# Kernel optimization log

Hardware: AMD Instinct MI355X
Metric: run time of the kernel (lower is better)

## Reference

```python
import jax, jax.numpy as jnp
import numpy as np

B, T, I, H, O = 256, 256, 128, 512, 1


def setup_inputs() -> dict:
    key = jax.random.key(0)
    ks = jax.random.split(key, 7)
    s = 1.0 / np.sqrt(H)  # torch default uniform-ish scale, use scaled normal
    return {
        "x": jax.random.normal(ks[0], (B, T, I), jnp.float32),
        "W_ih": jax.random.normal(ks[1], (H, I), jnp.float32) * s,
        "W_hh": jax.random.normal(ks[2], (H, H), jnp.float32) * s,
        "b_ih": jax.random.normal(ks[3], (H,), jnp.float32) * s,
        "b_hh": jax.random.normal(ks[4], (H,), jnp.float32) * s,
        "fc_w": jax.random.normal(ks[5], (O, H), jnp.float32) * s,
        "fc_b": jax.random.normal(ks[6], (O,), jnp.float32) * s,
    }


def reference(x, W_ih, W_hh, b_ih, b_hh, fc_w, fc_b):
    # Elman RNN (tanh), batch_first, h0 = 0; fc applied to last-step hidden.
    # Precompute all input projections in one big GEMM: [T, B, H]
    xs = jnp.einsum('bti,hi->tbh', x, W_ih) + (b_ih + b_hh)

    def step(h, xt):  # h: [B, H], xt: [B, H]
        h = jnp.tanh(xt + h @ W_hh.T)
        return h, None

    h0 = jnp.zeros((x.shape[0], W_hh.shape[0]), x.dtype)
    hT, _ = jax.lax.scan(step, h0, xs)
    return hT @ fc_w.T + fc_b  # [B, O]
```

## Files before the change

### kernel.cpp

```cpp
#include <hip/hip_runtime.h>


#define B_   256
#define T_   256
#define I_   128
#define H_   512

typedef __attribute__((ext_vector_type(8))) short short8;
typedef __attribute__((ext_vector_type(4))) float f32x4;

static __device__ inline unsigned short f2bf(float f) {
    union { float f; unsigned u; } v; v.f = f;
    unsigned r = v.u + 0x7fffu + ((v.u >> 16) & 1u);
    return (unsigned short)(r >> 16);
}
static __device__ inline float bf2f(unsigned short s) {
    union { unsigned u; float f; } v; v.u = ((unsigned)s) << 16;
    return v.f;
}
static __device__ inline float fast_tanh(float x) {
    float e = __expf(2.0f * x);
    float r = __builtin_amdgcn_rcpf(e + 1.0f);
    return __builtin_fmaf(-2.0f, r, 1.0f);
}
static __device__ inline short8 pack8(float4 lo, float4 hi) {
    short8 v;
    v[0] = (short)f2bf(lo.x); v[1] = (short)f2bf(lo.y);
    v[2] = (short)f2bf(lo.z); v[3] = (short)f2bf(lo.w);
    v[4] = (short)f2bf(hi.x); v[5] = (short)f2bf(hi.y);
    v[6] = (short)f2bf(hi.z); v[7] = (short)f2bf(hi.w);
    return v;
}

#define NKC   16
#define RS2  520
#define KC_LDS 3
#define KC_REG 3
#define KC_STR 10

__global__ void pack_w16(const float* __restrict__ W_hh,
                         unsigned short* __restrict__ Bpack) {
    int idx = blockIdx.x * blockDim.x + threadIdx.x;
    if (idx >= 32 * NKC * 64) return;
    int lane = idx & 63;
    int kc   = (idx >> 6) % NKC;
    int nt   = (idx >> 6) / NKC;
    int n  = nt * 16 + (lane & 15);
    int k0 = kc * 32 + (lane >> 4) * 8;
    unsigned short* dst = Bpack + (size_t)idx * 8;
#pragma unroll
    for (int e = 0; e < 8; ++e)
        dst[e] = f2bf(W_hh[n * H_ + k0 + e]);
}

__global__ __launch_bounds__(256)
void xproj_k(const float* __restrict__ x,
             const float* __restrict__ W_ih,
             const float* __restrict__ b_ih,
             const float* __restrict__ b_hh,
             unsigned short* __restrict__ xp) {
    const int tid  = threadIdx.x;
    const int lane = tid & 63;
    const int w    = tid >> 6;
    const int mr   = lane & 15;
    const int q    = lane >> 4;
    const int t0   = blockIdx.x * 4;
    const int bg   = blockIdx.y;

    short8 bf[4][4];
    const float* xb = x + (size_t)(16 * bg + mr) * T_ * I_ + q * 8;
#pragma unroll
    for (int tt = 0; tt < 4; ++tt)
#pragma unroll
        for (int kc = 0; kc < 4; ++kc) {
            const float* p = xb + (size_t)(t0 + tt) * I_ + kc * 32;
            bf[tt][kc] = pack8(*(const float4*)(p), *(const float4*)(p + 4));
        }

#pragma unroll
    for (int mt = 0; mt < 8; ++mt) {
        const int nrow = w * 128 + mt * 16 + mr;
        f32x4 a[4];
#pragma unroll
        for (int tt = 0; tt < 4; ++tt) a[tt] = (f32x4)(0.0f);
#pragma unroll
        for (int kc = 0; kc < 4; ++kc) {
            const float* ab = W_ih + (size_t)nrow * I_ + kc * 32 + q * 8;
            short8 af = pack8(*(const float4*)(ab), *(const float4*)(ab + 4));
#pragma unroll
            for (int tt = 0; tt < 4; ++tt)
                a[tt] = __builtin_amdgcn_mfma_f32_16x16x32_bf16(af, bf[tt][kc], a[tt], 0, 0, 0);
        }
#pragma unroll
        for (int tt = 0; tt < 4; ++tt) {
            unsigned short* dst = xp + ((size_t)((t0 + tt) * 16 + bg) * 512) * 16;
#pragma unroll
            for (int e = 0; e < 4; ++e) {
                int n = w * 128 + mt * 16 + q * 4 + e;
                float bv = b_ih[n] + b_hh[n];
                dst[(size_t)n * 16 + mr] = f2bf(a[tt][e] + bv);
            }
        }
    }
}

__global__ __launch_bounds__(512)
void rnn_fast(const unsigned short* __restrict__ Bpack,
              const unsigned short* __restrict__ xp,
              const float* __restrict__ fc_w,
              const float* __restrict__ fc_b,
              float* __restrict__ out) {
    __shared__ __align__(16) unsigned short a_lds[2][16 * RS2];
    __shared__ __align__(16) unsigned short w_lds[32 * KC_LDS * 64 * 8];

    const int tid  = threadIdx.x;
    const int lane = tid & 63;
    const int w    = tid >> 6;
    const int q    = lane >> 4;
    const int mr   = lane & 15;
    const int blk  = blockIdx.x;
    const int bb   = blk * 16;

    for (int i = tid; i < 16 * RS2; i += 512) a_lds[0][i] = 0;

    for (int i = tid; i < 32 * KC_LDS * 64; i += 512) {
        int l  = i & 63;
        int kc = (i >> 6) % KC_LDS;
        int nt = (i >> 6) / KC_LDS;
        *(short8*)&w_lds[(size_t)i * 8] =
            *(const short8*)(Bpack + ((size_t)(nt * NKC + kc) * 64 + l) * 8);
    }

    short8 wreg[KC_REG][4];
#pragma unroll
    for (int r = 0; r < KC_REG; ++r)
#pragma unroll
        for (int j = 0; j < 4; ++j)
            wreg[r][j] = *(const short8*)(Bpack +
                ((size_t)((4 * w + j) * NKC + KC_LDS + r) * 64 + lane) * 8);
#pragma unroll
    for (int r = 0; r < KC_REG; ++r)
#pragma unroll
        for (int j = 0; j < 4; ++j)
            asm volatile("" : "+v"(wreg[r][j]));

    __syncthreads();

    f32x4 acc[4];
    short8 sb[3][4];

    const unsigned short* xpt = xp + ((size_t)blk * 512) * 16;
    const size_t xstride = (size_t)16 * 512 * 16;

    for (int t = 0; t < T_; ++t) {
        const unsigned short* A = a_lds[t & 1];
        unsigned short* An      = a_lds[(t & 1) ^ 1];

#pragma unroll
        for (int s = 0; s < 3; ++s)
#pragma unroll
            for (int j = 0; j < 4; ++j)
                sb[s][j] = *(const short8*)(Bpack +
                    ((size_t)((4 * w + j) * NKC + KC_LDS + KC_REG + s) * 64 + lane) * 8);

        ushort4 xpr[4];
#pragma unroll
        for (int j = 0; j < 4; ++j) {
            int col = (4 * w + j) * 16 + mr;
            xpr[j] = *(const ushort4*)(xpt + (size_t)col * 16 + q * 4);
        }

#pragma unroll
        for (int j = 0; j < 4; ++j) acc[j] = (f32x4)(0.0f);

#pragma unroll
        for (int kc = 0; kc < KC_LDS; ++kc) {
            short8 af = *(const short8*)&A[mr * RS2 + kc * 32 + q * 8];
#pragma unroll
            for (int j = 0; j < 4; ++j) {
                short8 bfr = *(const short8*)&w_lds[
                    (size_t)(((4 * w + j) * KC_LDS + kc) * 64 + lane) * 8];
                acc[j] = __builtin_amdgcn_mfma_f32_16x16x32_bf16(af, bfr, acc[j], 0, 0, 0);
            }
        }
#pragma unroll
        for (int r = 0; r < KC_REG; ++r) {
            short8 af = *(const short8*)&A[mr * RS2 + (KC_LDS + r) * 32 + q * 8];
#pragma unroll
            for (int j = 0; j < 4; ++j)
                acc[j] = __builtin_amdgcn_mfma_f32_16x16x32_bf16(af, wreg[r][j], acc[j], 0, 0, 0);
        }
#pragma unroll
        for (int s = 0; s < KC_STR; ++s) {
            int kc = KC_LDS + KC_REG + s;
            short8 af = *(const short8*)&A[mr * RS2 + kc * 32 + q * 8];
#pragma unroll
            for (int j = 0; j < 4; ++j)
                acc[j] = __builtin_amdgcn_mfma_f32_16x16x32_bf16(af, sb[s % 3][j], acc[j], 0, 0, 0);
            if (s + 3 < KC_STR) {
#pragma unroll
                for (int j = 0; j < 4; ++j)
                    sb[s % 3][j] = *(const short8*)(Bpack +
                        ((size_t)((4 * w + j) * NKC + kc + 3) * 64 + lane) * 8);
            }
        }

#pragma unroll
        for (int j = 0; j < 4; ++j) {
            int col = (4 * w + j) * 16 + mr;
            const unsigned short* xj = (const unsigned short*)&xpr[j];
#pragma unroll
            for (int e = 0; e < 4; ++e) {
                float hv = fast_tanh(acc[j][e] + bf2f(xj[e]));
                An[(q * 4 + e) * RS2 + col] = f2bf(hv);
            }
        }
        xpt += xstride;
        __syncthreads();
    }

    {
        const int row = tid >> 5;
        const int l32 = tid & 31;
        float s = 0.0f;
        for (int k = l32; k < H_; k += 32)
            s += bf2f(a_lds[0][row * RS2 + k]) * fc_w[k];
#pragma unroll
        for (int off = 16; off > 0; off >>= 1)
            s += __shfl_down(s, off, 32);
        if (l32 == 0) out[bb + row] = s + fc_b[0];
    }
}

#define FB_NKC   20
#define FB_NKC_H 16
#define FB_RS   648
#define FB_KC_LDS 4
#define FB_KC_REG 5
#define FB_KC_STR 7

__global__ void pack_w20(const float* __restrict__ W_ih,
                         const float* __restrict__ W_hh,
                         unsigned short* __restrict__ Bpack) {
    int idx = blockIdx.x * blockDim.x + threadIdx.x;
    if (idx >= 32 * FB_NKC * 64) return;
    int lane = idx & 63;
    int kc   = (idx >> 6) % FB_NKC;
    int nt   = (idx >> 6) / FB_NKC;
    int n  = nt * 16 + (lane & 15);
    int k0 = kc * 32 + (lane >> 4) * 8;
    unsigned short* dst = Bpack + (size_t)idx * 8;
#pragma unroll
    for (int e = 0; e < 8; ++e) {
        int k = k0 + e;
        float v = (k < H_) ? W_hh[n * H_ + k] : W_ih[n * I_ + (k - H_)];
        dst[e] = f2bf(v);
    }
}

__global__ __launch_bounds__(512, 2)
void rnn_fb(const float* __restrict__ x,
            const unsigned short* __restrict__ Bpack,
            const float* __restrict__ b_ih,
            const float* __restrict__ b_hh,
            const float* __restrict__ fc_w,
            const float* __restrict__ fc_b,
            float* __restrict__ out) {
    __shared__ __align__(16) unsigned short a_lds[16 * FB_RS];
    __shared__ __align__(16) unsigned short w_lds[32 * FB_KC_LDS * 64 * 8];

    const int tid  = threadIdx.x;
    const int lane = tid & 63;
    const int w    = tid >> 6;
    const int q    = lane >> 4;
    const int mr   = lane & 15;
    const int bb   = blockIdx.x * 16;

    for (int i = tid; i < 16 * FB_RS; i += 512) a_lds[i] = 0;

    for (int i = tid; i < 32 * FB_KC_LDS * 64; i += 512) {
        int l  = i & 63;
        int kc = (i >> 6) & (FB_KC_LDS - 1);
        int nt = i >> 8;
        *(short8*)&w_lds[(size_t)i * 8] =
            *(const short8*)(Bpack + ((size_t)(nt * FB_NKC + kc) * 64 + l) * 8);
    }

    float bias[4];
#pragma unroll
    for (int j = 0; j < 4; ++j) {
        int col = (4 * w + j) * 16 + mr;
        bias[j] = b_ih[col] + b_hh[col];
    }

    short8 wih[4][4];
#pragma unroll
    for (int j = 0; j < 4; ++j)
#pragma unroll
        for (int kx = 0; kx < 4; ++kx)
            wih[j][kx] = *(const short8*)(Bpack +
                ((size_t)((4 * w + j) * FB_NKC + FB_NKC_H + kx) * 64 + lane) * 8);

    short8 wreg[FB_KC_REG][4];
#pragma unroll
    for (int r = 0; r < FB_KC_REG; ++r)
#pragma unroll
        for (int j = 0; j < 4; ++j)
            wreg[r][j] = *(const short8*)(Bpack +
                ((size_t)((4 * w + j) * FB_NKC + FB_KC_LDS + r) * 64 + lane) * 8);

    const int xrow = tid >> 5;
    const int xc   = (tid & 31) * 4;
    const float* xbase = x + (size_t)(bb + xrow) * T_ * I_ + xc;
    float4 xreg = *(const float4*)(xbase);

    __syncthreads();

    f32x4 acc[4];
    short8 sb[3][4];

    for (int t = 0; t < T_; ++t) {
#pragma unroll
        for (int s = 0; s < 3; ++s)
#pragma unroll
            for (int j = 0; j < 4; ++j)
                sb[s][j] = *(const short8*)(Bpack +
                    ((size_t)((4 * w + j) * FB_NKC + FB_KC_LDS + FB_KC_REG + s) * 64 + lane) * 8);

        {
            ushort4 xs;
            xs.x = f2bf(xreg.x); xs.y = f2bf(xreg.y);
            xs.z = f2bf(xreg.z); xs.w = f2bf(xreg.w);
            *(ushort4*)&a_lds[xrow * FB_RS + H_ + xc] = xs;
        }
        __syncthreads();

        if (t + 1 < T_)
            xreg = *(const float4*)(xbase + (size_t)(t + 1) * I_);

#pragma unroll
        for (int j = 0; j < 4; ++j) acc[j] = (f32x4)(0.0f);

#pragma unroll
        for (int kc = 0; kc < FB_KC_LDS; ++kc) {
            short8 af = *(const short8*)&a_lds[mr * FB_RS + kc * 32 + q * 8];
#pragma unroll
            for (int j = 0; j < 4; ++j) {
                short8 bfr = *(const short8*)&w_lds[
                    (size_t)(((4 * w + j) * FB_KC_LDS + kc) * 64 + lane) * 8];
                acc[j] = __builtin_amdgcn_mfma_f32_16x16x32_bf16(af, bfr, acc[j], 0, 0, 0);
            }
        }
#pragma unroll
        for (int r = 0; r < FB_KC_REG; ++r) {
            short8 af = *(const short8*)&a_lds[mr * FB_RS + (FB_KC_LDS + r) * 32 + q * 8];
#pragma unroll
            for (int j = 0; j < 4; ++j)
                acc[j] = __builtin_amdgcn_mfma_f32_16x16x32_bf16(af, wreg[r][j], acc[j], 0, 0, 0);
        }
#pragma unroll
        for (int kx = 0; kx < 4; ++kx) {
            short8 af = *(const short8*)&a_lds[mr * FB_RS + H_ + kx * 32 + q * 8];
#pragma unroll
            for (int j = 0; j < 4; ++j)
                acc[j] = __builtin_amdgcn_mfma_f32_16x16x32_bf16(af, wih[j][kx], acc[j], 0, 0, 0);
        }
#pragma unroll
        for (int s = 0; s < FB_KC_STR; ++s) {
            int kc = FB_KC_LDS + FB_KC_REG + s;
            short8 af = *(const short8*)&a_lds[mr * FB_RS + kc * 32 + q * 8];
#pragma unroll
            for (int j = 0; j < 4; ++j)
                acc[j] = __builtin_amdgcn_mfma_f32_16x16x32_bf16(af, sb[s % 3][j], acc[j], 0, 0, 0);
            if (s + 3 < FB_KC_STR) {
#pragma unroll
                for (int j = 0; j < 4; ++j)
                    sb[s % 3][j] = *(const short8*)(Bpack +
                        ((size_t)((4 * w + j) * FB_NKC + kc + 3) * 64 + lane) * 8);
            }
        }
        __syncthreads();

#pragma unroll
        for (int j = 0; j < 4; ++j) {
            int col = (4 * w + j) * 16 + mr;
#pragma unroll
            for (int e = 0; e < 4; ++e) {
                float hv = fast_tanh(acc[j][e] + bias[j]);
                a_lds[(q * 4 + e) * FB_RS + col] = f2bf(hv);
            }
        }
    }
    __syncthreads();

    {
        const int row = tid >> 5;
        const int l32 = tid & 31;
        float s = 0.0f;
        for (int k = l32; k < H_; k += 32)
            s += bf2f(a_lds[row * FB_RS + k]) * fc_w[k];
#pragma unroll
        for (int off = 16; off > 0; off >>= 1)
            s += __shfl_down(s, off, 32);
        if (l32 == 0) out[bb + row] = s + fc_b[0];
    }
}


extern "C" void kernel_launch(void* const* d_in, const int* in_sizes, int n_in,
                              void* d_out, int out_size, void* d_ws, size_t ws_size,
                              hipStream_t stream) {
    const float* x    = (const float*)d_in[0];
    const float* W_ih = (const float*)d_in[1];
    const float* W_hh = (const float*)d_in[2];
    const float* b_ih = (const float*)d_in[3];
    const float* b_hh = (const float*)d_in[4];
    const float* fc_w = (const float*)d_in[5];
    const float* fc_b = (const float*)d_in[6];

    const size_t XP_OFF    = (size_t)32 * NKC * 64 * 8 * 2;
    const size_t NEED_FAST = XP_OFF + (size_t)T_ * H_ * B_ * 2;

    if (ws_size >= NEED_FAST) {
        unsigned short* Bpack = (unsigned short*)d_ws;
        unsigned short* xp = (unsigned short*)((char*)d_ws + XP_OFF);
        pack_w16<<<128, 256, 0, stream>>>(W_hh, Bpack);
        xproj_k<<<dim3(T_ / 4, 16), 256, 0, stream>>>(x, W_ih, b_ih, b_hh, xp);
        rnn_fast<<<16, 512, 0, stream>>>(Bpack, xp, fc_w, fc_b, (float*)d_out);
    } else {
        unsigned short* Bpack = (unsigned short*)d_ws;
        pack_w20<<<160, 256, 0, stream>>>(W_ih, W_hh, Bpack);
        rnn_fb<<<16, 512, 0, stream>>>(x, Bpack, b_ih, b_hh, fc_w, fc_b, (float*)d_out);
    }
}
```

Before: 649.7 us.

## Rebalance W_hh residency, XOR-swizzle hidden-state LDS, and prepack W_ih

The recurrent kernel now keeps more W_hh k-chunks resident in LDS and in registers, so fewer chunks are streamed from global memory on every timestep. The padded hidden-state LDS row stride is replaced by an unpadded layout with an XOR swizzle to avoid bank conflicts. Register-budget attributes are added so the larger register-resident weight set fits. W_ih is also prepacked to bf16 MFMA layout with a precomputed combined bias, which removes repeated fp32 conversion in the projection kernel; the catch is an extra small launch and higher register pressure that could cause spills.

Result: slower. 970.1 us (+49.3%).

```diff
diff --git a/kernel.cpp b/kernel.cpp
--- a/kernel.cpp
+++ b/kernel.cpp
@@ -33,10 +33,10 @@
 }
 
 #define NKC   16
-#define RS2  520
-#define KC_LDS 3
-#define KC_REG 3
-#define KC_STR 10
+#define RS3  512
+#define KC_LDS 4
+#define KC_REG 8
+#define KC_STR 4
 
 __global__ void pack_w16(const float* __restrict__ W_hh,
                          unsigned short* __restrict__ Bpack) {
@@ -53,11 +53,30 @@
         dst[e] = f2bf(W_hh[n * H_ + k0 + e]);
 }
 
+__global__ void pack_wia(const float* __restrict__ W_ih,
+                         const float* __restrict__ b_ih,
+                         const float* __restrict__ b_hh,
+                         unsigned short* __restrict__ wia,
+                         float* __restrict__ bv) {
+    int idx = blockIdx.x * blockDim.x + threadIdx.x;
+    if (idx < 32 * 4 * 64) {
+        int lane = idx & 63;
+        int kc   = (idx >> 6) & 3;
+        int nt   = idx >> 8;
+        int row  = nt * 16 + (lane & 15);
+        int k0   = kc * 32 + (lane >> 4) * 8;
+        unsigned short* dst = wia + (size_t)idx * 8;
+#pragma unroll
+        for (int e = 0; e < 8; ++e)
+            dst[e] = f2bf(W_ih[row * I_ + k0 + e]);
+    }
+    if (idx < H_) bv[idx] = b_ih[idx] + b_hh[idx];
+}
+
 __global__ __launch_bounds__(256)
 void xproj_k(const float* __restrict__ x,
-             const float* __restrict__ W_ih,
-             const float* __restrict__ b_ih,
-             const float* __restrict__ b_hh,
+             const unsigned short* __restrict__ wia,
+             const float* __restrict__ bv,
              unsigned short* __restrict__ xp) {
     const int tid  = threadIdx.x;
     const int lane = tid & 63;
@@ -79,14 +98,13 @@
 
 #pragma unroll
     for (int mt = 0; mt < 8; ++mt) {
-        const int nrow = w * 128 + mt * 16 + mr;
+        const int nt = w * 8 + mt;
         f32x4 a[4];
 #pragma unroll
         for (int tt = 0; tt < 4; ++tt) a[tt] = (f32x4)(0.0f);
 #pragma unroll
         for (int kc = 0; kc < 4; ++kc) {
-            const float* ab = W_ih + (size_t)nrow * I_ + kc * 32 + q * 8;
-            short8 af = pack8(*(const float4*)(ab), *(const float4*)(ab + 4));
+            short8 af = *(const short8*)&wia[((size_t)(nt * 4 + kc) * 64 + lane) * 8];
 #pragma unroll
             for (int tt = 0; tt < 4; ++tt)
                 a[tt] = __builtin_amdgcn_mfma_f32_16x16x32_bf16(af, bf[tt][kc], a[tt], 0, 0, 0);
@@ -96,21 +114,23 @@
             unsigned short* dst = xp + ((size_t)((t0 + tt) * 16 + bg) * 512) * 16;
 #pragma unroll
             for (int e = 0; e < 4; ++e) {
-                int n = w * 128 + mt * 16 + q * 4 + e;
-                float bv = b_ih[n] + b_hh[n];
-                dst[(size_t)n * 16 + mr] = f2bf(a[tt][e] + bv);
-            }
-        }
-    }
-}
-
-__global__ __launch_bounds__(512)
+                int n = nt * 16 + q * 4 + e;
+                dst[(size_t)n * 16 + mr] = f2bf(a[tt][e] + bv[n]);
+            }
+        }
+    }
+}
+
+__global__
+__launch_bounds__(512, 2)
+__attribute__((amdgpu_waves_per_eu(2, 2)))
+__attribute__((amdgpu_num_vgpr(248)))
 void rnn_fast(const unsigned short* __restrict__ Bpack,
               const unsigned short* __restrict__ xp,
               const float* __restrict__ fc_w,
               const float* __restrict__ fc_b,
               float* __restrict__ out) {
-    __shared__ __align__(16) unsigned short a_lds[2][16 * RS2];
+    __shared__ __align__(16) unsigned short a_lds[2][16 * RS3];
     __shared__ __align__(16) unsigned short w_lds[32 * KC_LDS * 64 * 8];
 
     const int tid  = threadIdx.x;
@@ -121,7 +141,7 @@
     const int blk  = blockIdx.x;
     const int bb   = blk * 16;
 
-    for (int i = tid; i < 16 * RS2; i += 512) a_lds[0][i] = 0;
+    for (int i = tid; i < 16 * RS3; i += 512) a_lds[0][i] = 0;
 
     for (int i = tid; i < 32 * KC_LDS * 64; i += 512) {
         int l  = i & 63;
@@ -149,6 +169,8 @@
     f32x4 acc[4];
     short8 sb[3][4];
 
+    const int akey = (mr & 7) << 3;
+
     const unsigned short* xpt = xp + ((size_t)blk * 512) * 16;
     const size_t xstride = (size_t)16 * 512 * 16;
 
@@ -175,7 +197,7 @@
 
 #pragma unroll
         for (int kc = 0; kc < KC_LDS; ++kc) {
-            short8 af = *(const short8*)&A[mr * RS2 + kc * 32 + q * 8];
+            short8 af = *(const short8*)&A[mr * RS3 + ((kc * 32 + q * 8) ^ akey)];
 #pragma unroll
             for (int j = 0; j < 4; ++j) {
                 short8 bfr = *(const short8*)&w_lds[
@@ -185,7 +207,8 @@
         }
 #pragma unroll
         for (int r = 0; r < KC_REG; ++r) {
-            short8 af = *(const short8*)&A[mr * RS2 + (KC_LDS + r) * 32 + q * 8];
+            short8 af = *(const short8*)&A[mr * RS3 +
+                (((KC_LDS + r) * 32 + q * 8) ^ akey)];
 #pragma unroll
             for (int j = 0; j < 4; ++j)
                 acc[j] = __builtin_amdgcn_mfma_f32_16x16x32_bf16(af, wreg[r][j], acc[j], 0, 0, 0);
@@ -193,7 +216,7 @@
 #pragma unroll
         for (int s = 0; s < KC_STR; ++s) {
             int kc = KC_LDS + KC_REG + s;
-            short8 af = *(const short8*)&A[mr * RS2 + kc * 32 + q * 8];
+            short8 af = *(const short8*)&A[mr * RS3 + ((kc * 32 + q * 8) ^ akey)];
 #pragma unroll
             for (int j = 0; j < 4; ++j)
                 acc[j] = __builtin_amdgcn_mfma_f32_16x16x32_bf16(af, sb[s % 3][j], acc[j], 0, 0, 0);
@@ -211,8 +234,9 @@
             const unsigned short* xj = (const unsigned short*)&xpr[j];
 #pragma unroll
             for (int e = 0; e < 4; ++e) {
+                int row = q * 4 + e;
                 float hv = fast_tanh(acc[j][e] + bf2f(xj[e]));
-                An[(q * 4 + e) * RS2 + col] = f2bf(hv);
+                An[row * RS3 + (col ^ ((row & 7) << 3))] = f2bf(hv);
             }
         }
         xpt += xstride;
@@ -222,9 +246,10 @@
     {
         const int row = tid >> 5;
         const int l32 = tid & 31;
+        const int fkey = (row & 7) << 3;
         float s = 0.0f;
         for (int k = l32; k < H_; k += 32)
-            s += bf2f(a_lds[0][row * RS2 + k]) * fc_w[k];
+            s += bf2f(a_lds[0][row * RS3 + (k ^ fkey)]) * fc_w[k];
 #pragma unroll
         for (int off = 16; off > 0; off >>= 1)
             s += __shfl_down(s, off, 32);
@@ -418,14 +443,20 @@
     const float* fc_w = (const float*)d_in[5];
     const float* fc_b = (const float*)d_in[6];
 
-    const size_t XP_OFF    = (size_t)32 * NKC * 64 * 8 * 2;
+    const size_t BP_SZ  = (size_t)32 * NKC * 64 * 8 * 2;
+    const size_t WIA_SZ = (size_t)32 * 4 * 64 * 8 * 2;
+    const size_t BV_SZ  = (size_t)H_ * 4;
+    const size_t XP_OFF = BP_SZ + WIA_SZ + BV_SZ;
     const size_t NEED_FAST = XP_OFF + (size_t)T_ * H_ * B_ * 2;
 
     if (ws_size >= NEED_FAST) {
         unsigned short* Bpack = (unsigned short*)d_ws;
-        unsigned short* xp = (unsigned short*)((char*)d_ws + XP_OFF);
+        unsigned short* wia   = (unsigned short*)((char*)d_ws + BP_SZ);
+        float*          bv    = (float*)((char*)d_ws + BP_SZ + WIA_SZ);
+        unsigned short* xp    = (unsigned short*)((char*)d_ws + XP_OFF);
         pack_w16<<<128, 256, 0, stream>>>(W_hh, Bpack);
-        xproj_k<<<dim3(T_ / 4, 16), 256, 0, stream>>>(x, W_ih, b_ih, b_hh, xp);
+        pack_wia<<<32, 256, 0, stream>>>(W_ih, b_ih, b_hh, wia, bv);
+        xproj_k<<<dim3(T_ / 4, 16), 256, 0, stream>>>(x, wia, bv, xp);
         rnn_fast<<<16, 512, 0, stream>>>(Bpack, xp, fc_w, fc_b, (float*)d_out);
     } else {
         unsigned short* Bpack = (unsigned short*)d_ws;
```
